# Optimization experiments

Measured on AMD Instinct MI355X. Metric: run time of the kernel, lower is better.

## Reference

```python
import jax, jax.numpy as jnp
import numpy as np

N = 100000   # nodes
E = 1600000  # edges (before self-loops)
C = 128      # num_node_features == graph_hidden_channels (residuals require equality)
NHID = 512
NOUT = 256
B = 512      # number of graphs in the batch
BN_EPS = 1e-5


def setup_inputs() -> dict:
    key = jax.random.key(0)
    ks = list(jax.random.split(key, 32))
    k = iter(ks)

    def w(shape, fan_in):
        return jax.random.normal(next(k), shape, jnp.float32) * (1.0 / np.sqrt(fan_in))

    inp = {}
    inp["x"] = jax.random.normal(next(k), (N, C), jnp.float32)
    inp["edge_index"] = jax.random.randint(next(k), (2, E), 0, N, jnp.int32)
    inp["batch"] = jnp.sort(jax.random.randint(next(k), (N,), 0, B, jnp.int32))
    # three GCN layers: lin weight [C,C], bias [C], BN gamma/beta
    for i in (1, 2, 3):
        inp[f"W{i}"] = w((C, C), C)
        inp[f"b{i}"] = jnp.zeros((C,), jnp.float32)
        inp[f"g{i}"] = jnp.ones((C,), jnp.float32)
        inp[f"be{i}"] = jnp.zeros((C,), jnp.float32)
    # GAT (1 head)
    inp["Wa"] = w((C, C), C)
    inp["asrc"] = w((C,), C)
    inp["adst"] = w((C,), C)
    inp["ba"] = jnp.zeros((C,), jnp.float32)
    inp["ga"] = jnp.ones((C,), jnp.float32)
    inp["bea"] = jnp.zeros((C,), jnp.float32)
    # MLP head
    inp["Wh1"] = w((C, NHID), C)
    inp["bh1"] = jnp.zeros((NHID,), jnp.float32)
    inp["Wm0"] = w((NHID, NHID), NHID)
    inp["bm0"] = jnp.zeros((NHID,), jnp.float32)
    inp["Wm1"] = w((NHID, NHID), NHID)
    inp["bm1"] = jnp.zeros((NHID,), jnp.float32)
    inp["Wo"] = w((NHID, NOUT), NHID)
    inp["bo"] = jnp.zeros((NOUT,), jnp.float32)
    return inp


def _add_self_loops(edge_index):
    loops = jnp.arange(N, dtype=edge_index.dtype)
    src = jnp.concatenate([edge_index[0], loops])
    dst = jnp.concatenate([edge_index[1], loops])
    return src, dst


def _gcn(x, src, dst, W, b):
    # PyG GCNConv: add self-loops, D^-1/2 (A+I) D^-1/2 (x W) + b
    deg = jax.ops.segment_sum(jnp.ones_like(dst, jnp.float32), dst, num_segments=N)
    dinv = jax.lax.rsqrt(jnp.maximum(deg, 1.0))
    norm = dinv[src] * dinv[dst]                      # [E+N]
    h = x @ W                                         # [N,C]
    msg = h[src] * norm[:, None]                      # gather + scale
    return jax.ops.segment_sum(msg, dst, num_segments=N) + b


def _gat(x, src, dst, W, asrc, adst, b):
    # PyG GATConv, heads=1: self-loops, alpha = softmax_dst(leaky_relu(a_s.h_j + a_d.h_i))
    h = x @ W                                         # [N,C]
    es = (h * asrc).sum(-1)                           # [N]
    ed = (h * adst).sum(-1)
    e = jax.nn.leaky_relu(es[src] + ed[dst], 0.2)     # [E+N]
    m = jax.ops.segment_max(e, dst, num_segments=N)
    ex = jnp.exp(e - m[dst])
    s = jax.ops.segment_sum(ex, dst, num_segments=N)
    alpha = ex / (s[dst] + 1e-16)
    out = jax.ops.segment_sum(h[src] * alpha[:, None], dst, num_segments=N)
    return out + b


def _bn(h, g, be):
    # BatchNorm in training mode: biased batch stats over node dim
    m = h.mean(0)
    v = ((h - m) ** 2).mean(0)
    return (h - m) * jax.lax.rsqrt(v + BN_EPS) * g + be


def reference(x, edge_index, batch,
              W1, b1, g1, be1, W2, b2, g2, be2, W3, b3, g3, be3,
              Wa, asrc, adst, ba, ga, bea,
              Wh1, bh1, Wm0, bm0, Wm1, bm1, Wo, bo):
    src, dst = _add_self_loops(edge_index)
    x = jax.nn.relu(_bn(_gcn(x, src, dst, W1, b1), g1, be1)) + x
    x = jax.nn.relu(_bn(_gcn(x, src, dst, W2, b2), g2, be2)) + x
    x = jax.nn.relu(_bn(_gcn(x, src, dst, W3, b3), g3, be3)) + x
    x = jax.nn.relu(_bn(_gat(x, src, dst, Wa, asrc, adst, ba), ga, bea)) + x
    # global mean pool over graphs
    sums = jax.ops.segment_sum(x, batch, num_segments=B)
    cnt = jax.ops.segment_sum(jnp.ones((N,), jnp.float32), batch, num_segments=B)
    x = sums / jnp.maximum(cnt, 1.0)[:, None]         # [B,C]
    x = jax.nn.relu(x @ Wh1 + bh1)
    x = jax.nn.relu(x @ Wm0 + bm0)
    x = jax.nn.relu(x @ Wm1 + bm1)
    return x @ Wo + bo                                # [B,NOUT]
```

## Files before the change

kernel.cpp:

```cpp
#include <hip/hip_runtime.h>

#define N_NODES 100000
#define N_EDGES 1600000
#define CCH     128
#define BG      512
#define NHID    512
#define NOUT    256
#define BN_EPS  1e-5f

typedef __attribute__((ext_vector_type(8))) short s16x8;
typedef __attribute__((ext_vector_type(4))) float f32x4;

static __device__ __forceinline__ float leaky(float x) { return x > 0.f ? x : 0.2f * x; }
static __device__ __forceinline__ uint32_t bfr16(float x) {
  uint32_t u = __float_as_uint(x);
  u += 0x7fffu + ((u >> 16) & 1u);
  return u >> 16;
}
static __device__ __forceinline__ uint32_t pack2(float a, float b) {
  return bfr16(a) | (bfr16(b) << 16);
}
static __device__ __forceinline__ float blo(uint32_t u) { return __uint_as_float(u << 16); }
static __device__ __forceinline__ float bhi(uint32_t u) { return __uint_as_float(u & 0xffff0000u); }

__global__ void hist_kernel(const int* __restrict__ dst, int* __restrict__ indeg) {
  int e = blockIdx.x * 256 + threadIdx.x;
  if (e < N_EDGES) atomicAdd(&indeg[dst[e]], 1);
}

__global__ __launch_bounds__(256) void scan_chunks(const int* __restrict__ indeg,
                                                   int* __restrict__ rowstart,
                                                   int* __restrict__ chunksum) {
  int tid = threadIdx.x;
  int base = blockIdx.x * 1024 + tid * 4;
  int4 v;
  if (base + 3 < N_NODES) {
    v = *(const int4*)(indeg + base);
  } else {
    v.x = (base + 0 < N_NODES) ? indeg[base + 0] : 0;
    v.y = (base + 1 < N_NODES) ? indeg[base + 1] : 0;
    v.z = (base + 2 < N_NODES) ? indeg[base + 2] : 0;
    v.w = (base + 3 < N_NODES) ? indeg[base + 3] : 0;
  }
  int s = v.x + v.y + v.z + v.w;
  __shared__ int ss[256];
  ss[tid] = s;
  __syncthreads();
  for (int off = 1; off < 256; off <<= 1) {
    int t = (tid >= off) ? ss[tid - off] : 0;
    __syncthreads();
    ss[tid] += t;
    __syncthreads();
  }
  int excl = ss[tid] - s;
  if (base + 0 < N_NODES) rowstart[base + 0] = excl;
  if (base + 1 < N_NODES) rowstart[base + 1] = excl + v.x;
  if (base + 2 < N_NODES) rowstart[base + 2] = excl + v.x + v.y;
  if (base + 3 < N_NODES) rowstart[base + 3] = excl + v.x + v.y + v.z;
  if (tid == 255) chunksum[blockIdx.x] = ss[255];
}

__global__ void scan_sums(int* __restrict__ chunksum, int nch) {
  __shared__ int ss[128];
  int tid = threadIdx.x;
  int v = (tid < nch) ? chunksum[tid] : 0;
  ss[tid] = v;
  __syncthreads();
  for (int off = 1; off < 128; off <<= 1) {
    int t = (tid >= off) ? ss[tid - off] : 0;
    __syncthreads();
    ss[tid] += t;
    __syncthreads();
  }
  if (tid < nch) chunksum[tid] = ss[tid] - v;
}

__global__ void scan_add(int* __restrict__ rowstart, const int* __restrict__ chunksum) {
  int i = blockIdx.x * 256 + threadIdx.x;
  if (i < N_NODES)      rowstart[i] += chunksum[i >> 10];
  else if (i == N_NODES) rowstart[N_NODES] = N_EDGES;
}

__global__ void compute_dinv(const int* __restrict__ indeg, float* __restrict__ dinv) {
  int i = blockIdx.x * 256 + threadIdx.x;
  if (i < N_NODES) dinv[i] = rsqrtf((float)(indeg[i] + 1));
}

__global__ void scatter_edges(const int* __restrict__ src, const int* __restrict__ dst,
                              const int* __restrict__ rowstart, int* __restrict__ cursor,
                              const float* __restrict__ dinv, int2* __restrict__ csr_sw) {
  int e = blockIdx.x * 256 + threadIdx.x;
  if (e < N_EDGES) {
    int d = dst[e];
    int s = src[e];
    int p = rowstart[d] + atomicAdd(&cursor[d], 1);
    float w = dinv[s] * dinv[d];
    csr_sw[p] = make_int2(s, __float_as_int(w));
  }
}

__global__ void cast_bf16_kernel(const float2* __restrict__ x2, uint32_t* __restrict__ xb) {
  size_t idx = (size_t)blockIdx.x * 256 + threadIdx.x;
  if (idx >= (size_t)N_NODES * 64) return;
  float2 v = x2[idx];
  xb[idx] = pack2(v.x, v.y);
}

__global__ void pack_w_kernel(const float* __restrict__ W, unsigned short* __restrict__ Wp) {
  int t = blockIdx.x * 256 + threadIdx.x;
  if (t >= 2048) return;
  int lane = t & 63;
  int ks = (t >> 6) & 3;
  int nt = t >> 8;
  int c = nt * 16 + (lane & 15);
  int kb = ks * 32 + (lane >> 4) * 8;
#pragma unroll
  for (int i = 0; i < 8; ++i)
    Wp[(size_t)t * 8 + i] = (unsigned short)bfr16(W[(size_t)(kb + i) * 128 + c]);
}

__global__ __launch_bounds__(256) void gemm_mfma(const uint32_t* __restrict__ Ab,
                                                 const unsigned short* __restrict__ Wp,
                                                 uint32_t* __restrict__ Hb,
                                                 int M) {
  int wave = threadIdx.x >> 6, lane = threadIdx.x & 63;
  int row0 = blockIdx.x * 128 + wave * 32;
  const unsigned short* A16 = (const unsigned short*)Ab;

  f32x4 acc[2][8];
#pragma unroll
  for (int mt = 0; mt < 2; ++mt)
#pragma unroll
    for (int nt = 0; nt < 8; ++nt) acc[mt][nt] = (f32x4){0.f, 0.f, 0.f, 0.f};

  s16x8 a[2][4];
  int r = lane & 15, ko = (lane >> 4) * 8;
#pragma unroll
  for (int mt = 0; mt < 2; ++mt) {
    int row = row0 + mt * 16 + r;
    bool v = row < M;
    const unsigned short* ap = A16 + (size_t)row * 128 + ko;
#pragma unroll
    for (int ks = 0; ks < 4; ++ks) {
      s16x8 af = {0, 0, 0, 0, 0, 0, 0, 0};
      if (v) af = *(const s16x8*)(ap + ks * 32);
      a[mt][ks] = af;
    }
  }
#pragma unroll
  for (int ks = 0; ks < 4; ++ks) {
#pragma unroll
    for (int nt = 0; nt < 8; ++nt) {
      s16x8 b = *(const s16x8*)(Wp + ((size_t)(nt * 4 + ks) * 64 + lane) * 8);
      acc[0][nt] = __builtin_amdgcn_mfma_f32_16x16x32_bf16(a[0][ks], b, acc[0][nt], 0, 0, 0);
      acc[1][nt] = __builtin_amdgcn_mfma_f32_16x16x32_bf16(a[1][ks], b, acc[1][nt], 0, 0, 0);
    }
  }
#pragma unroll
  for (int mt = 0; mt < 2; ++mt) {
#pragma unroll
    for (int nt = 0; nt < 8; ++nt) {
#pragma unroll
      for (int reg = 0; reg < 4; ++reg) {
        float v0 = acc[mt][nt][reg];
        float v1 = __shfl_xor(v0, 1);
        int row = row0 + mt * 16 + (lane >> 4) * 4 + reg;
        int col = nt * 16 + (lane & 15);
        if (!(lane & 1) && row < M)
          Hb[(size_t)row * 64 + (col >> 1)] = pack2(v0, v1);
      }
    }
  }
}

template <int GAT>
__global__ __launch_bounds__(256) void agg_kernel(const uint2* __restrict__ Hb2,
                                                  const int* __restrict__ rowstart,
                                                  const int2* __restrict__ pack,
                                                  const float* __restrict__ dinv,
                                                  const float* __restrict__ wselfa,
                                                  const float* __restrict__ winv,
                                                  float4* __restrict__ agg4,
                                                  float* __restrict__ stats) {
  int tid = threadIdx.x;
  int lane = tid & 63;
  int hl = lane & 31;
  int half = lane >> 5;
  int gw = (blockIdx.x * 256 + tid) >> 6;
  int nw = (gridDim.x * 256) >> 6;
  float s0 = 0, s1 = 0, s2 = 0, s3 = 0, q0 = 0, q1 = 0, q2 = 0, q3 = 0;
  for (int pi = gw; pi < N_NODES / 2; pi += nw) {
    int n = 2 * pi + half;
    int e0 = rowstart[n], e1 = rowstart[n + 1];
    int len = e1 - e0;
    int G = (len + 3) >> 2;
    int Gmax = max(G, __shfl_xor(G, 32));
    int ecl = (len > 0) ? (e1 - 1) : 0;
    float selfw, fscale;
    if (GAT) { selfw = wselfa[n]; fscale = winv[n]; }
    else     { float di = dinv[n]; selfw = di * di; fscale = 1.f; }
    uint2 hs = Hb2[(size_t)n * 32 + hl];
    float c0 = blo(hs.x) * selfw, c1 = bhi(hs.x) * selfw;
    float c2 = blo(hs.y) * selfw, c3 = bhi(hs.y) * selfw;

    if (Gmax > 0) {
      uint2 rA0, rA1, rA2, rA3;
      float wA0, wA1, wA2, wA3;
      int iB0, iB1, iB2, iB3;
      float wB0 = 0, wB1 = 0, wB2 = 0, wB3 = 0;
      iB0 = iB1 = iB2 = iB3 = 0;
      {
        int e = e0;
        int2 pa = pack[e < e1 ? e : ecl];
        int2 pb = pack[e + 1 < e1 ? e + 1 : ecl];
        int2 pc = pack[e + 2 < e1 ? e + 2 : ecl];
        int2 pd = pack[e + 3 < e1 ? e + 3 : ecl];
        wA0 = (e < e1) ? __int_as_float(pa.y) : 0.f;
        wA1 = (e + 1 < e1) ? __int_as_float(pb.y) : 0.f;
        wA2 = (e + 2 < e1) ? __int_as_float(pc.y) : 0.f;
        wA3 = (e + 3 < e1) ? __int_as_float(pd.y) : 0.f;
        rA0 = Hb2[(size_t)pa.x * 32 + hl];
        rA1 = Hb2[(size_t)pb.x * 32 + hl];
        rA2 = Hb2[(size_t)pc.x * 32 + hl];
        rA3 = Hb2[(size_t)pd.x * 32 + hl];
      }
      if (Gmax > 1) {
        int e = e0 + 4;
        int2 pa = pack[e < e1 ? e : ecl];
        int2 pb = pack[e + 1 < e1 ? e + 1 : ecl];
        int2 pc = pack[e + 2 < e1 ? e + 2 : ecl];
        int2 pd = pack[e + 3 < e1 ? e + 3 : ecl];
        iB0 = pa.x; wB0 = (e < e1) ? __int_as_float(pa.y) : 0.f;
        iB1 = pb.x; wB1 = (e + 1 < e1) ? __int_as_float(pb.y) : 0.f;
        iB2 = pc.x; wB2 = (e + 2 < e1) ? __int_as_float(pc.y) : 0.f;
        iB3 = pd.x; wB3 = (e + 3 < e1) ? __int_as_float(pd.y) : 0.f;
      }
      for (int g = 0; g < Gmax; ++g) {
        uint2 rB0, rB1, rB2, rB3;
        int nI0, nI1, nI2, nI3;
        float nw0, nw1, nw2, nw3;
        if (g + 1 < Gmax) {
          rB0 = Hb2[(size_t)iB0 * 32 + hl];
          rB1 = Hb2[(size_t)iB1 * 32 + hl];
          rB2 = Hb2[(size_t)iB2 * 32 + hl];
          rB3 = Hb2[(size_t)iB3 * 32 + hl];
        }
        if (g + 2 < Gmax) {
          int e = e0 + (g + 2) * 4;
          int2 pa = pack[e < e1 ? e : ecl];
          int2 pb = pack[e + 1 < e1 ? e + 1 : ecl];
          int2 pc = pack[e + 2 < e1 ? e + 2 : ecl];
          int2 pd = pack[e + 3 < e1 ? e + 3 : ecl];
          nI0 = pa.x; nw0 = (e < e1) ? __int_as_float(pa.y) : 0.f;
          nI1 = pb.x; nw1 = (e + 1 < e1) ? __int_as_float(pb.y) : 0.f;
          nI2 = pc.x; nw2 = (e + 2 < e1) ? __int_as_float(pc.y) : 0.f;
          nI3 = pd.x; nw3 = (e + 3 < e1) ? __int_as_float(pd.y) : 0.f;
        }
        c0 = fmaf(blo(rA0.x), wA0, c0); c1 = fmaf(bhi(rA0.x), wA0, c1);
        c2 = fmaf(blo(rA0.y), wA0, c2); c3 = fmaf(bhi(rA0.y), wA0, c3);
        c0 = fmaf(blo(rA1.x), wA1, c0); c1 = fmaf(bhi(rA1.x), wA1, c1);
        c2 = fmaf(blo(rA1.y), wA1, c2); c3 = fmaf(bhi(rA1.y), wA1, c3);
        c0 = fmaf(blo(rA2.x), wA2, c0); c1 = fmaf(bhi(rA2.x), wA2, c1);
        c2 = fmaf(blo(rA2.y), wA2, c2); c3 = fmaf(bhi(rA2.y), wA2, c3);
        c0 = fmaf(blo(rA3.x), wA3, c0); c1 = fmaf(bhi(rA3.x), wA3, c1);
        c2 = fmaf(blo(rA3.y), wA3, c2); c3 = fmaf(bhi(rA3.y), wA3, c3);
        rA0 = rB0; rA1 = rB1; rA2 = rB2; rA3 = rB3;
        wA0 = wB0; wA1 = wB1; wA2 = wB2; wA3 = wB3;
        iB0 = nI0; iB1 = nI1; iB2 = nI2; iB3 = nI3;
        wB0 = nw0; wB1 = nw1; wB2 = nw2; wB3 = nw3;
      }
    }
    if (GAT) { c0 *= fscale; c1 *= fscale; c2 *= fscale; c3 *= fscale; }
    agg4[(size_t)n * 32 + hl] = make_float4(c0, c1, c2, c3);
    s0 += c0; s1 += c1; s2 += c2; s3 += c3;
    q0 += c0 * c0; q1 += c1 * c1; q2 += c2 * c2; q3 += c3 * c3;
  }
  s0 += __shfl_xor(s0, 32); s1 += __shfl_xor(s1, 32);
  s2 += __shfl_xor(s2, 32); s3 += __shfl_xor(s3, 32);
  q0 += __shfl_xor(q0, 32); q1 += __shfl_xor(q1, 32);
  q2 += __shfl_xor(q2, 32); q3 += __shfl_xor(q3, 32);
  __shared__ float red[4][128];
  int w = tid >> 6;
  if (half == 0) {
    red[w][4 * hl + 0] = s0; red[w][4 * hl + 1] = s1;
    red[w][4 * hl + 2] = s2; red[w][4 * hl + 3] = s3;
  }
  __syncthreads();
  if (w == 0) {
    float a = red[0][2 * lane] + red[1][2 * lane] + red[2][2 * lane] + red[3][2 * lane];
    float b = red[0][2 * lane + 1] + red[1][2 * lane + 1] + red[2][2 * lane + 1] + red[3][2 * lane + 1];
    atomicAdd(&stats[2 * lane], a);
    atomicAdd(&stats[2 * lane + 1], b);
  }
  __syncthreads();
  if (half == 0) {
    red[w][4 * hl + 0] = q0; red[w][4 * hl + 1] = q1;
    red[w][4 * hl + 2] = q2; red[w][4 * hl + 3] = q3;
  }
  __syncthreads();
  if (w == 0) {
    float a = red[0][2 * lane] + red[1][2 * lane] + red[2][2 * lane] + red[3][2 * lane];
    float b = red[0][2 * lane + 1] + red[1][2 * lane + 1] + red[2][2 * lane + 1] + red[3][2 * lane + 1];
    atomicAdd(&stats[128 + 2 * lane], a);
    atomicAdd(&stats[128 + 2 * lane + 1], b);
  }
}

__global__ __launch_bounds__(256) void compute_esed(const uint32_t* __restrict__ Hb,
                                                    const float* __restrict__ asrc,
                                                    const float* __restrict__ adst,
                                                    float* __restrict__ es, float* __restrict__ ed) {
  int lane = threadIdx.x & 63;
  int gwave = (blockIdx.x * 256 + threadIdx.x) >> 6;
  if (gwave >= N_NODES) return;
  float2 av = ((const float2*)asrc)[lane];
  float2 dv = ((const float2*)adst)[lane];
  uint32_t hv = Hb[(size_t)gwave * 64 + lane];
  float hx = blo(hv), hy = bhi(hv);
  float e_s = hx * av.x + hy * av.y;
  float e_d = hx * dv.x + hy * dv.y;
  for (int off = 32; off; off >>= 1) {
    e_s += __shfl_down(e_s, off);
    e_d += __shfl_down(e_d, off);
  }
  if (lane == 0) { es[gwave] = e_s; ed[gwave] = e_d; }
}

__global__ void gat_prep_node(int2* __restrict__ pack, const int* __restrict__ rowstart,
                              const float* __restrict__ es, const float* __restrict__ ed,
                              float* __restrict__ wselfa, float* __restrict__ winv) {
  int n = blockIdx.x * 256 + threadIdx.x;
  if (n >= N_NODES) return;
  int e0 = rowstart[n], e1 = rowstart[n + 1];
  float edi = ed[n];
  float wself = __expf(leaky(es[n] + edi));
  float s = wself;
  for (int e = e0; e < e1; ++e) {
    int sidx = pack[e].x;
    float w = __expf(leaky(es[sidx] + edi));
    pack[e].y = __float_as_int(w);
    s += w;
  }
  wselfa[n] = wself;
  winv[n] = 1.f / (s + 1e-16f);
}

__global__ void bn_relu_res(const float4* __restrict__ agg4, const float* __restrict__ stats,
                            const float* __restrict__ gamma, const float* __restrict__ beta,
                            uint2* __restrict__ xb) {
  size_t idx = (size_t)blockIdx.x * 256 + threadIdx.x;
  if (idx >= (size_t)N_NODES * 32) return;
  int c = ((int)(idx & 31)) * 4;
  const float n_inv = 1.f / (float)N_NODES;
  float sc[4], bc[4];
#pragma unroll
  for (int k = 0; k < 4; ++k) {
    float m = stats[c + k] * n_inv;
    float v = stats[128 + c + k] * n_inv - m * m;
    sc[k] = gamma[c + k] * rsqrtf(v + BN_EPS);
    bc[k] = beta[c + k] - m * sc[k];
  }
  float4 a = agg4[idx];
  uint2 xi = xb[idx];
  float r0 = fmaxf(fmaf(a.x, sc[0], bc[0]), 0.f) + blo(xi.x);
  float r1 = fmaxf(fmaf(a.y, sc[1], bc[1]), 0.f) + bhi(xi.x);
  float r2 = fmaxf(fmaf(a.z, sc[2], bc[2]), 0.f) + blo(xi.y);
  float r3 = fmaxf(fmaf(a.w, sc[3], bc[3]), 0.f) + bhi(xi.y);
  xb[idx] = make_uint2(pack2(r0, r1), pack2(r2, r3));
}

__global__ void graph_starts(const int* __restrict__ batch, int* __restrict__ gstart) {
  int n = blockIdx.x * 256 + threadIdx.x;
  if (n >= N_NODES) return;
  int b = batch[n];
  int bp = (n == 0) ? -1 : batch[n - 1];
  for (int g = bp + 1; g <= b; ++g) gstart[g] = n;
  if (n == N_NODES - 1) {
    for (int g = b + 1; g <= BG; ++g) gstart[g] = N_NODES;
  }
}

__global__ __launch_bounds__(256) void pool_kernel(const uint32_t* __restrict__ xb,
                                                   const int* __restrict__ gstart,
                                                   float* __restrict__ pooled) {
  int g = blockIdx.x;
  int c = threadIdx.x & 127;
  int half = threadIdx.x >> 7;
  int s = gstart[g], e = gstart[g + 1];
  float acc = 0.f;
  for (int n = s + half; n < e; n += 2) {
    uint32_t u = xb[(size_t)n * 64 + (c >> 1)];
    acc += (c & 1) ? bhi(u) : blo(u);
  }
  __shared__ float red[256];
  red[threadIdx.x] = acc;
  __syncthreads();
  if (half == 0) {
    float v = red[c] + red[128 + c];
    int cnt = e - s;
    pooled[(size_t)g * 128 + c] = v / fmaxf((float)cnt, 1.f);
  }
}

template <int RELU, int BIAS>
__global__ __launch_bounds__(256) void gemm_f32(const float* __restrict__ A,
                                                const float* __restrict__ W,
                                                const float* __restrict__ bias,
                                                float* __restrict__ Cmat,
                                                int M, int K, int N) {
  __shared__ float As[32][128];
  __shared__ float Bs[32][128];
  int tid = threadIdx.x;
  int row0 = blockIdx.x * 128, col0 = blockIdx.y * 128;
  int tx = tid & 15, ty = tid >> 4;
  float acc[8][8];
#pragma unroll
  for (int i = 0; i < 8; ++i)
#pragma unroll
    for (int j = 0; j < 8; ++j) acc[i][j] = 0.f;

  for (int k0 = 0; k0 < K; k0 += 32) {
    {
      int r = tid >> 1;
      int kseg = (tid & 1) * 16;
      bool valid = (row0 + r) < M;
      const float* ap = A + (size_t)(row0 + r) * K + k0 + kseg;
#pragma unroll
      for (int q = 0; q < 4; ++q) {
        float4 v;
        if (valid) v = *(const float4*)(ap + q * 4);
        else { v.x = v.y = v.z = v.w = 0.f; }
        As[kseg + q * 4 + 0][r] = v.x;
        As[kseg + q * 4 + 1][r] = v.y;
        As[kseg + q * 4 + 2][r] = v.z;
        As[kseg + q * 4 + 3][r] = v.w;
      }
    }
    {
      int kk = tid >> 3;
      int seg = (tid & 7) * 16;
      const float* wp = W + (size_t)(k0 + kk) * N + col0 + seg;
#pragma unroll
      for (int q = 0; q < 4; ++q)
        *(float4*)&Bs[kk][seg + q * 4] = *(const float4*)(wp + q * 4);
    }
    __syncthreads();
#pragma unroll
    for (int kk = 0; kk < 32; ++kk) {
      float4 a0 = *(const float4*)&As[kk][ty * 4];
      float4 a1 = *(const float4*)&As[kk][64 + ty * 4];
      float4 b0 = *(const float4*)&Bs[kk][tx * 4];
      float4 b1 = *(const float4*)&Bs[kk][64 + tx * 4];
      float av[8] = {a0.x, a0.y, a0.z, a0.w, a1.x, a1.y, a1.z, a1.w};
      float bv[8] = {b0.x, b0.y, b0.z, b0.w, b1.x, b1.y, b1.z, b1.w};
#pragma unroll
      for (int i = 0; i < 8; ++i)
#pragma unroll
        for (int j = 0; j < 8; ++j) acc[i][j] = fmaf(av[i], bv[j], acc[i][j]);
    }
    __syncthreads();
  }
#pragma unroll
  for (int i = 0; i < 8; ++i) {
    int r = row0 + ((i < 4) ? (ty * 4 + i) : (64 + ty * 4 + i - 4));
    if (r >= M) continue;
#pragma unroll
    for (int j = 0; j < 8; ++j) {
      int c = col0 + ((j < 4) ? (tx * 4 + j) : (64 + tx * 4 + j - 4));
      float v = acc[i][j];
      if (BIAS) v += bias[c];
      if (RELU) v = fmaxf(v, 0.f);
      Cmat[(size_t)r * N + c] = v;
    }
  }
}

extern "C" void kernel_launch(void* const* d_in, const int* in_sizes, int n_in,
                              void* d_out, int out_size, void* d_ws, size_t ws_size,
                              hipStream_t stream) {
  const float* x_in  = (const float*)d_in[0];
  const int*   eidx  = (const int*)d_in[1];
  const int*   batch = (const int*)d_in[2];
  const float* W1 = (const float*)d_in[3];
  const float* g1 = (const float*)d_in[5];
  const float* be1 = (const float*)d_in[6];
  const float* W2 = (const float*)d_in[7];
  const float* g2 = (const float*)d_in[9];
  const float* be2 = (const float*)d_in[10];
  const float* W3 = (const float*)d_in[11];
  const float* g3 = (const float*)d_in[13];
  const float* be3 = (const float*)d_in[14];
  const float* Wa = (const float*)d_in[15];
  const float* asrc = (const float*)d_in[16];
  const float* adst = (const float*)d_in[17];
  const float* ga = (const float*)d_in[19];
  const float* bea = (const float*)d_in[20];
  const float* Wh1 = (const float*)d_in[21];
  const float* bh1 = (const float*)d_in[22];
  const float* Wm0 = (const float*)d_in[23];
  const float* bm0 = (const float*)d_in[24];
  const float* Wm1 = (const float*)d_in[25];
  const float* bm1 = (const float*)d_in[26];
  const float* Wo = (const float*)d_in[27];
  const float* bo = (const float*)d_in[28];

  const int* src = eidx;
  const int* dst = eidx + N_EDGES;

  char* p = (char*)d_ws;
  auto alloc = [&](size_t bytes) {
    char* r = p;
    p += (bytes + 255) & ~(size_t)255;
    return r;
  };
  uint32_t* Hb     = (uint32_t*)alloc((size_t)N_NODES * 64 * 4);
  uint32_t* xb     = (uint32_t*)alloc((size_t)N_NODES * 64 * 4);
  float* agg       = (float*)alloc((size_t)N_NODES * CCH * 4);
  int2*  csr_sw    = (int2*)alloc((size_t)N_EDGES * 8);
  int*   rowstart  = (int*)alloc((size_t)(N_NODES + 1) * 4);
  int*   indeg     = (int*)alloc((size_t)2 * N_NODES * 4);
  int*   cursor    = indeg + N_NODES;
  float* dinv      = (float*)alloc((size_t)N_NODES * 4);
  float* es        = (float*)alloc((size_t)N_NODES * 4);
  float* ed        = (float*)alloc((size_t)N_NODES * 4);
  float* wselfa    = (float*)alloc((size_t)N_NODES * 4);
  float* winv      = (float*)alloc((size_t)N_NODES * 4);
  int*   chunksum  = (int*)alloc(128 * 4);
  float* stats     = (float*)alloc(4 * 256 * 4);
  int*   gstart    = (int*)alloc((BG + 1) * 4);
  float* pooled    = (float*)alloc((size_t)BG * CCH * 4);
  float* m1        = (float*)alloc((size_t)BG * NHID * 4);
  float* m2        = (float*)alloc((size_t)BG * NHID * 4);
  unsigned short* Wp1 = (unsigned short*)alloc(2048 * 8 * 2);
  unsigned short* Wp2 = (unsigned short*)alloc(2048 * 8 * 2);
  unsigned short* Wp3 = (unsigned short*)alloc(2048 * 8 * 2);
  unsigned short* Wp4 = (unsigned short*)alloc(2048 * 8 * 2);

  hipMemsetAsync(indeg, 0, (size_t)2 * N_NODES * 4, stream);
  hipMemsetAsync(stats, 0, 4 * 256 * 4, stream);

  hist_kernel<<<(N_EDGES + 255) / 256, 256, 0, stream>>>(dst, indeg);
  scan_chunks<<<98, 256, 0, stream>>>(indeg, rowstart, chunksum);
  scan_sums<<<1, 128, 0, stream>>>(chunksum, 98);
  scan_add<<<(N_NODES + 256) / 256, 256, 0, stream>>>(rowstart, chunksum);
  compute_dinv<<<(N_NODES + 255) / 256, 256, 0, stream>>>(indeg, dinv);
  scatter_edges<<<(N_EDGES + 255) / 256, 256, 0, stream>>>(src, dst, rowstart, cursor, dinv, csr_sw);

  const int el2_blocks = (N_NODES * 64 + 255) / 256;
  const int el4_blocks = (N_NODES * 32 + 255) / 256;
  cast_bf16_kernel<<<el2_blocks, 256, 0, stream>>>((const float2*)x_in, xb);
  pack_w_kernel<<<8, 256, 0, stream>>>(W1, Wp1);
  pack_w_kernel<<<8, 256, 0, stream>>>(W2, Wp2);
  pack_w_kernel<<<8, 256, 0, stream>>>(W3, Wp3);
  pack_w_kernel<<<8, 256, 0, stream>>>(Wa, Wp4);

  const int gemm_blocks_m = (N_NODES + 127) / 128;
  const int AGG_BLOCKS = 2048;

  const unsigned short* Wps[3] = {Wp1, Wp2, Wp3};
  const float* gs[3] = {g1, g2, g3};
  const float* bes[3] = {be1, be2, be3};
  for (int l = 0; l < 3; ++l) {
    gemm_mfma<<<gemm_blocks_m, 256, 0, stream>>>(xb, Wps[l], Hb, N_NODES);
    agg_kernel<0><<<AGG_BLOCKS, 256, 0, stream>>>((const uint2*)Hb, rowstart, csr_sw, dinv,
                                                  nullptr, nullptr, (float4*)agg, stats + l * 256);
    bn_relu_res<<<el4_blocks, 256, 0, stream>>>((const float4*)agg, stats + l * 256,
                                                gs[l], bes[l], (uint2*)xb);
  }

  gemm_mfma<<<gemm_blocks_m, 256, 0, stream>>>(xb, Wp4, Hb, N_NODES);
  compute_esed<<<(N_NODES + 3) / 4, 256, 0, stream>>>(Hb, asrc, adst, es, ed);
  gat_prep_node<<<(N_NODES + 255) / 256, 256, 0, stream>>>(csr_sw, rowstart, es, ed, wselfa, winv);
  agg_kernel<1><<<AGG_BLOCKS, 256, 0, stream>>>((const uint2*)Hb, rowstart, csr_sw, nullptr,
                                                wselfa, winv, (float4*)agg, stats + 3 * 256);
  bn_relu_res<<<el4_blocks, 256, 0, stream>>>((const float4*)agg, stats + 3 * 256,
                                              ga, bea, (uint2*)xb);

  graph_starts<<<(N_NODES + 255) / 256, 256, 0, stream>>>(batch, gstart);
  pool_kernel<<<BG, 256, 0, stream>>>(xb, gstart, pooled);

  gemm_f32<1, 1><<<dim3(4, 4), 256, 0, stream>>>(pooled, Wh1, bh1, m1, BG, CCH, NHID);
  gemm_f32<1, 1><<<dim3(4, 4), 256, 0, stream>>>(m1, Wm0, bm0, m2, BG, NHID, NHID);
  gemm_f32<1, 1><<<dim3(4, 4), 256, 0, stream>>>(m2, Wm1, bm1, m1, BG, NHID, NHID);
  gemm_f32<0, 1><<<dim3(4, 2), 256, 0, stream>>>(m1, Wo, bo, (float*)d_out, BG, NHID, NOUT);
}
```

Before: 1.201 ms.

## Fuse BN/ReLU/residual into GEMM prologue and pooling, restructure GAT weights

Folds the BatchNorm+ReLU+residual pass into the next layer's MFMA GEMM prologue, and the last one into the pooling kernel, so the separate elementwise kernel that re-read agg and xb is gone. The GAT edge-weight prep is now a per-edge pass that stores es[src]. The aggregation kernel computes the exp/leaky weights and softmax denominator inline, which costs a second pass over each row's edges. Small setup kernels (scan_add with dinv, input cast with weight packing) are merged to cut launch count.

```diff
diff --git a/kernel.cpp b/kernel.cpp
--- a/kernel.cpp
+++ b/kernel.cpp
@@ -75,15 +75,15 @@
   if (tid < nch) chunksum[tid] = ss[tid] - v;
 }
 
-__global__ void scan_add(int* __restrict__ rowstart, const int* __restrict__ chunksum) {
+__global__ void scan_add_dinv(int* __restrict__ rowstart, const int* __restrict__ chunksum,
+                              const int* __restrict__ indeg, float* __restrict__ dinv) {
   int i = blockIdx.x * 256 + threadIdx.x;
-  if (i < N_NODES)      rowstart[i] += chunksum[i >> 10];
-  else if (i == N_NODES) rowstart[N_NODES] = N_EDGES;
-}
-
-__global__ void compute_dinv(const int* __restrict__ indeg, float* __restrict__ dinv) {
-  int i = blockIdx.x * 256 + threadIdx.x;
-  if (i < N_NODES) dinv[i] = rsqrtf((float)(indeg[i] + 1));
+  if (i < N_NODES) {
+    rowstart[i] += chunksum[i >> 10];
+    dinv[i] = rsqrtf((float)(indeg[i] + 1));
+  } else if (i == N_NODES) {
+    rowstart[N_NODES] = N_EDGES;
+  }
 }
 
 __global__ void scatter_edges(const int* __restrict__ src, const int* __restrict__ dst,
@@ -99,16 +99,23 @@
   }
 }
 
-__global__ void cast_bf16_kernel(const float2* __restrict__ x2, uint32_t* __restrict__ xb) {
-  size_t idx = (size_t)blockIdx.x * 256 + threadIdx.x;
-  if (idx >= (size_t)N_NODES * 64) return;
-  float2 v = x2[idx];
-  xb[idx] = pack2(v.x, v.y);
-}
-
-__global__ void pack_w_kernel(const float* __restrict__ W, unsigned short* __restrict__ Wp) {
-  int t = blockIdx.x * 256 + threadIdx.x;
-  if (t >= 2048) return;
+__global__ void prep_kernel(const float2* __restrict__ x2, uint32_t* __restrict__ xb,
+                            const float* __restrict__ W1, const float* __restrict__ W2,
+                            const float* __restrict__ W3, const float* __restrict__ W4,
+                            unsigned short* __restrict__ Wp1, unsigned short* __restrict__ Wp2,
+                            unsigned short* __restrict__ Wp3, unsigned short* __restrict__ Wp4) {
+  int b = blockIdx.x;
+  if (b < 25000) {
+    size_t idx = (size_t)b * 256 + threadIdx.x;
+    float2 v = x2[idx];
+    xb[idx] = pack2(v.x, v.y);
+    return;
+  }
+  int pb = b - 25000;
+  int wsel = pb >> 3;
+  int t = (pb & 7) * 256 + threadIdx.x;
+  const float* W = (wsel == 0) ? W1 : (wsel == 1) ? W2 : (wsel == 2) ? W3 : W4;
+  unsigned short* Wp = (wsel == 0) ? Wp1 : (wsel == 1) ? Wp2 : (wsel == 2) ? Wp3 : Wp4;
   int lane = t & 63;
   int ks = (t >> 6) & 3;
   int nt = t >> 8;
@@ -119,13 +126,31 @@
     Wp[(size_t)t * 8 + i] = (unsigned short)bfr16(W[(size_t)(kb + i) * 128 + c]);
 }
 
-__global__ __launch_bounds__(256) void gemm_mfma(const uint32_t* __restrict__ Ab,
+template <int FUSE>
+__global__ __launch_bounds__(256) void gemm_mfma(uint32_t* __restrict__ xbm,
+                                                 const float* __restrict__ aggf,
+                                                 const float* __restrict__ stats,
+                                                 const float* __restrict__ gamma,
+                                                 const float* __restrict__ beta,
                                                  const unsigned short* __restrict__ Wp,
                                                  uint32_t* __restrict__ Hb,
                                                  int M) {
+  __shared__ float scs[128], bcs[128];
+  if (FUSE) {
+    int t = threadIdx.x;
+    if (t < 128) {
+      const float n_inv = 1.f / (float)N_NODES;
+      float m = stats[t] * n_inv;
+      float v = stats[128 + t] * n_inv - m * m;
+      float s = gamma[t] * rsqrtf(v + BN_EPS);
+      scs[t] = s;
+      bcs[t] = beta[t] - m * s;
+    }
+    __syncthreads();
+  }
   int wave = threadIdx.x >> 6, lane = threadIdx.x & 63;
   int row0 = blockIdx.x * 128 + wave * 32;
-  const unsigned short* A16 = (const unsigned short*)Ab;
+  int r = lane & 15, g = lane >> 4;
 
   f32x4 acc[2][8];
 #pragma unroll
@@ -134,26 +159,52 @@
     for (int nt = 0; nt < 8; ++nt) acc[mt][nt] = (f32x4){0.f, 0.f, 0.f, 0.f};
 
   s16x8 a[2][4];
-  int r = lane & 15, ko = (lane >> 4) * 8;
 #pragma unroll
   for (int mt = 0; mt < 2; ++mt) {
     int row = row0 + mt * 16 + r;
     bool v = row < M;
-    const unsigned short* ap = A16 + (size_t)row * 128 + ko;
-#pragma unroll
-    for (int ks = 0; ks < 4; ++ks) {
-      s16x8 af = {0, 0, 0, 0, 0, 0, 0, 0};
-      if (v) af = *(const s16x8*)(ap + ks * 32);
-      a[mt][ks] = af;
+    if (FUSE) {
+#pragma unroll
+      for (int ks = 0; ks < 4; ++ks) {
+        int ch = ks * 32 + g * 8;
+        s16x8 af = {0, 0, 0, 0, 0, 0, 0, 0};
+        if (v) {
+          const float4* ap = (const float4*)(aggf + (size_t)row * 128 + ch);
+          float4 a0 = ap[0], a1 = ap[1];
+          uint4 xo = *(const uint4*)(xbm + (size_t)row * 64 + (ch >> 1));
+          float aa[8] = {a0.x, a0.y, a0.z, a0.w, a1.x, a1.y, a1.z, a1.w};
+          float xold[8] = {blo(xo.x), bhi(xo.x), blo(xo.y), bhi(xo.y),
+                           blo(xo.z), bhi(xo.z), blo(xo.w), bhi(xo.w)};
+          uint32_t pk[4];
+#pragma unroll
+          for (int jj = 0; jj < 4; ++jj) {
+            float r0v = fmaxf(fmaf(aa[2 * jj],     scs[ch + 2 * jj],     bcs[ch + 2 * jj]),     0.f) + xold[2 * jj];
+            float r1v = fmaxf(fmaf(aa[2 * jj + 1], scs[ch + 2 * jj + 1], bcs[ch + 2 * jj + 1]), 0.f) + xold[2 * jj + 1];
+            pk[jj] = pack2(r0v, r1v);
+          }
+          uint4 st = make_uint4(pk[0], pk[1], pk[2], pk[3]);
+          *(uint4*)(xbm + (size_t)row * 64 + (ch >> 1)) = st;
+          af = *(s16x8*)&st;
+        }
+        a[mt][ks] = af;
+      }
+    } else {
+      const unsigned short* ap = (const unsigned short*)xbm + (size_t)row * 128 + g * 8;
+#pragma unroll
+      for (int ks = 0; ks < 4; ++ks) {
+        s16x8 af = {0, 0, 0, 0, 0, 0, 0, 0};
+        if (v) af = *(const s16x8*)(ap + ks * 32);
+        a[mt][ks] = af;
+      }
     }
   }
 #pragma unroll
   for (int ks = 0; ks < 4; ++ks) {
 #pragma unroll
     for (int nt = 0; nt < 8; ++nt) {
-      s16x8 b = *(const s16x8*)(Wp + ((size_t)(nt * 4 + ks) * 64 + lane) * 8);
-      acc[0][nt] = __builtin_amdgcn_mfma_f32_16x16x32_bf16(a[0][ks], b, acc[0][nt], 0, 0, 0);
-      acc[1][nt] = __builtin_amdgcn_mfma_f32_16x16x32_bf16(a[1][ks], b, acc[1][nt], 0, 0, 0);
+      s16x8 bfr = *(const s16x8*)(Wp + ((size_t)(nt * 4 + ks) * 64 + lane) * 8);
+      acc[0][nt] = __builtin_amdgcn_mfma_f32_16x16x32_bf16(a[0][ks], bfr, acc[0][nt], 0, 0, 0);
+      acc[1][nt] = __builtin_amdgcn_mfma_f32_16x16x32_bf16(a[1][ks], bfr, acc[1][nt], 0, 0, 0);
     }
   }
 #pragma unroll
@@ -178,8 +229,8 @@
                                                   const int* __restrict__ rowstart,
                                                   const int2* __restrict__ pack,
                                                   const float* __restrict__ dinv,
-                                                  const float* __restrict__ wselfa,
-                                                  const float* __restrict__ winv,
+                                                  const float* __restrict__ es,
+                                                  const float* __restrict__ ed,
                                                   float4* __restrict__ agg4,
                                                   float* __restrict__ stats) {
   int tid = threadIdx.x;
@@ -196,9 +247,23 @@
     int G = (len + 3) >> 2;
     int Gmax = max(G, __shfl_xor(G, 32));
     int ecl = (len > 0) ? (e1 - 1) : 0;
-    float selfw, fscale;
-    if (GAT) { selfw = wselfa[n]; fscale = winv[n]; }
-    else     { float di = dinv[n]; selfw = di * di; fscale = 1.f; }
+    float edi = 0.f, selfw, fscale = 1.f;
+    if (GAT) {
+      edi = ed[n];
+      float wself = __expf(leaky(es[n] + edi));
+      float wsum = (hl == 0) ? wself : 0.f;
+      for (int e = e0 + hl; e < e1; e += 32)
+        wsum += __expf(leaky(__int_as_float(pack[e].y) + edi));
+#pragma unroll
+      for (int off = 16; off; off >>= 1) wsum += __shfl_xor(wsum, off);
+      fscale = 1.f / (wsum + 1e-16f);
+      selfw = wself;
+    } else {
+      float di = dinv[n];
+      selfw = di * di;
+    }
+#define EDGEW(py, ok) (GAT ? ((ok) ? __expf(leaky(__int_as_float(py) + edi)) : 0.f) \
+                           : ((ok) ? __int_as_float(py) : 0.f))
     uint2 hs = Hb2[(size_t)n * 32 + hl];
     float c0 = blo(hs.x) * selfw, c1 = bhi(hs.x) * selfw;
     float c2 = blo(hs.y) * selfw, c3 = bhi(hs.y) * selfw;
@@ -206,19 +271,18 @@
     if (Gmax > 0) {
       uint2 rA0, rA1, rA2, rA3;
       float wA0, wA1, wA2, wA3;
-      int iB0, iB1, iB2, iB3;
+      int iB0 = 0, iB1 = 0, iB2 = 0, iB3 = 0;
       float wB0 = 0, wB1 = 0, wB2 = 0, wB3 = 0;
-      iB0 = iB1 = iB2 = iB3 = 0;
       {
         int e = e0;
         int2 pa = pack[e < e1 ? e : ecl];
         int2 pb = pack[e + 1 < e1 ? e + 1 : ecl];
         int2 pc = pack[e + 2 < e1 ? e + 2 : ecl];
         int2 pd = pack[e + 3 < e1 ? e + 3 : ecl];
-        wA0 = (e < e1) ? __int_as_float(pa.y) : 0.f;
-        wA1 = (e + 1 < e1) ? __int_as_float(pb.y) : 0.f;
-        wA2 = (e + 2 < e1) ? __int_as_float(pc.y) : 0.f;
-        wA3 = (e + 3 < e1) ? __int_as_float(pd.y) : 0.f;
+        wA0 = EDGEW(pa.y, e < e1);
+        wA1 = EDGEW(pb.y, e + 1 < e1);
+        wA2 = EDGEW(pc.y, e + 2 < e1);
+        wA3 = EDGEW(pd.y, e + 3 < e1);
         rA0 = Hb2[(size_t)pa.x * 32 + hl];
         rA1 = Hb2[(size_t)pb.x * 32 + hl];
         rA2 = Hb2[(size_t)pc.x * 32 + hl];
@@ -230,10 +294,10 @@
         int2 pb = pack[e + 1 < e1 ? e + 1 : ecl];
         int2 pc = pack[e + 2 < e1 ? e + 2 : ecl];
         int2 pd = pack[e + 3 < e1 ? e + 3 : ecl];
-        iB0 = pa.x; wB0 = (e < e1) ? __int_as_float(pa.y) : 0.f;
-        iB1 = pb.x; wB1 = (e + 1 < e1) ? __int_as_float(pb.y) : 0.f;
-        iB2 = pc.x; wB2 = (e + 2 < e1) ? __int_as_float(pc.y) : 0.f;
-        iB3 = pd.x; wB3 = (e + 3 < e1) ? __int_as_float(pd.y) : 0.f;
+        iB0 = pa.x; wB0 = EDGEW(pa.y, e < e1);
+        iB1 = pb.x; wB1 = EDGEW(pb.y, e + 1 < e1);
+        iB2 = pc.x; wB2 = EDGEW(pc.y, e + 2 < e1);
+        iB3 = pd.x; wB3 = EDGEW(pd.y, e + 3 < e1);
       }
       for (int g = 0; g < Gmax; ++g) {
         uint2 rB0, rB1, rB2, rB3;
@@ -251,10 +315,10 @@
           int2 pb = pack[e + 1 < e1 ? e + 1 : ecl];
           int2 pc = pack[e + 2 < e1 ? e + 2 : ecl];
           int2 pd = pack[e + 3 < e1 ? e + 3 : ecl];
-          nI0 = pa.x; nw0 = (e < e1) ? __int_as_float(pa.y) : 0.f;
-          nI1 = pb.x; nw1 = (e + 1 < e1) ? __int_as_float(pb.y) : 0.f;
-          nI2 = pc.x; nw2 = (e + 2 < e1) ? __int_as_float(pc.y) : 0.f;
-          nI3 = pd.x; nw3 = (e + 3 < e1) ? __int_as_float(pd.y) : 0.f;
+          nI0 = pa.x; nw0 = EDGEW(pa.y, e < e1);
+          nI1 = pb.x; nw1 = EDGEW(pb.y, e + 1 < e1);
+          nI2 = pc.x; nw2 = EDGEW(pc.y, e + 2 < e1);
+          nI3 = pd.x; nw3 = EDGEW(pd.y, e + 3 < e1);
         }
         c0 = fmaf(blo(rA0.x), wA0, c0); c1 = fmaf(bhi(rA0.x), wA0, c1);
         c2 = fmaf(blo(rA0.y), wA0, c2); c3 = fmaf(bhi(rA0.y), wA0, c3);
@@ -270,6 +334,7 @@
         wB0 = nw0; wB1 = nw1; wB2 = nw2; wB3 = nw3;
       }
     }
+#undef EDGEW
     if (GAT) { c0 *= fscale; c1 *= fscale; c2 *= fscale; c3 *= fscale; }
     agg4[(size_t)n * 32 + hl] = make_float4(c0, c1, c2, c3);
     s0 += c0; s1 += c1; s2 += c2; s3 += c3;
@@ -326,47 +391,13 @@
   if (lane == 0) { es[gwave] = e_s; ed[gwave] = e_d; }
 }
 
-__global__ void gat_prep_node(int2* __restrict__ pack, const int* __restrict__ rowstart,
-                              const float* __restrict__ es, const float* __restrict__ ed,
-                              float* __restrict__ wselfa, float* __restrict__ winv) {
-  int n = blockIdx.x * 256 + threadIdx.x;
-  if (n >= N_NODES) return;
-  int e0 = rowstart[n], e1 = rowstart[n + 1];
-  float edi = ed[n];
-  float wself = __expf(leaky(es[n] + edi));
-  float s = wself;
-  for (int e = e0; e < e1; ++e) {
-    int sidx = pack[e].x;
-    float w = __expf(leaky(es[sidx] + edi));
-    pack[e].y = __float_as_int(w);
-    s += w;
-  }
-  wselfa[n] = wself;
-  winv[n] = 1.f / (s + 1e-16f);
-}
-
-__global__ void bn_relu_res(const float4* __restrict__ agg4, const float* __restrict__ stats,
-                            const float* __restrict__ gamma, const float* __restrict__ beta,
-                            uint2* __restrict__ xb) {
-  size_t idx = (size_t)blockIdx.x * 256 + threadIdx.x;
-  if (idx >= (size_t)N_NODES * 32) return;
-  int c = ((int)(idx & 31)) * 4;
-  const float n_inv = 1.f / (float)N_NODES;
-  float sc[4], bc[4];
-#pragma unroll
-  for (int k = 0; k < 4; ++k) {
-    float m = stats[c + k] * n_inv;
-    float v = stats[128 + c + k] * n_inv - m * m;
-    sc[k] = gamma[c + k] * rsqrtf(v + BN_EPS);
-    bc[k] = beta[c + k] - m * sc[k];
-  }
-  float4 a = agg4[idx];
-  uint2 xi = xb[idx];
-  float r0 = fmaxf(fmaf(a.x, sc[0], bc[0]), 0.f) + blo(xi.x);
-  float r1 = fmaxf(fmaf(a.y, sc[1], bc[1]), 0.f) + bhi(xi.x);
-  float r2 = fmaxf(fmaf(a.z, sc[2], bc[2]), 0.f) + blo(xi.y);
-  float r3 = fmaxf(fmaf(a.w, sc[3], bc[3]), 0.f) + bhi(xi.y);
-  xb[idx] = make_uint2(pack2(r0, r1), pack2(r2, r3));
+__global__ void gat_pack_kernel(int2* __restrict__ sw, const float* __restrict__ es) {
+  int e = blockIdx.x * 256 + threadIdx.x;
+  if (e < N_EDGES) {
+    int2 v = sw[e];
+    v.y = __float_as_int(es[v.x]);
+    sw[e] = v;
+  }
 }
 
 __global__ void graph_starts(const int* __restrict__ batch, int* __restrict__ gstart) {
@@ -380,25 +411,36 @@
   }
 }
 
-__global__ __launch_bounds__(256) void pool_kernel(const uint32_t* __restrict__ xb,
-                                                   const int* __restrict__ gstart,
-                                                   float* __restrict__ pooled) {
+__global__ __launch_bounds__(256) void pool_bn(const float* __restrict__ aggf,
+                                               const uint32_t* __restrict__ xb,
+                                               const float* __restrict__ stats,
+                                               const float* __restrict__ gamma,
+                                               const float* __restrict__ beta,
+                                               const int* __restrict__ gstart,
+                                               float* __restrict__ pooled) {
   int g = blockIdx.x;
   int c = threadIdx.x & 127;
   int half = threadIdx.x >> 7;
+  const float n_inv = 1.f / (float)N_NODES;
+  float m = stats[c] * n_inv;
+  float v = stats[128 + c] * n_inv - m * m;
+  float sc = gamma[c] * rsqrtf(v + BN_EPS);
+  float bc = beta[c] - m * sc;
   int s = gstart[g], e = gstart[g + 1];
   float acc = 0.f;
   for (int n = s + half; n < e; n += 2) {
+    float a = aggf[(size_t)n * 128 + c];
     uint32_t u = xb[(size_t)n * 64 + (c >> 1)];
-    acc += (c & 1) ? bhi(u) : blo(u);
+    float xo = (c & 1) ? bhi(u) : blo(u);
+    acc += fmaxf(fmaf(a, sc, bc), 0.f) + xo;
   }
   __shared__ float red[256];
   red[threadIdx.x] = acc;
   __syncthreads();
   if (half == 0) {
-    float v = red[c] + red[128 + c];
+    float vsum = red[c] + red[128 + c];
     int cnt = e - s;
-    pooled[(size_t)g * 128 + c] = v / fmaxf((float)cnt, 1.f);
+    pooled[(size_t)g * 128 + c] = vsum / fmaxf((float)cnt, 1.f);
   }
 }
 
@@ -523,8 +565,6 @@
   float* dinv      = (float*)alloc((size_t)N_NODES * 4);
   float* es        = (float*)alloc((size_t)N_NODES * 4);
   float* ed        = (float*)alloc((size_t)N_NODES * 4);
-  float* wselfa    = (float*)alloc((size_t)N_NODES * 4);
-  float* winv      = (float*)alloc((size_t)N_NODES * 4);
   int*   chunksum  = (int*)alloc(128 * 4);
   float* stats     = (float*)alloc(4 * 256 * 4);
   int*   gstart    = (int*)alloc((BG + 1) * 4);
@@ -542,42 +582,36 @@
   hist_kernel<<<(N_EDGES + 255) / 256, 256, 0, stream>>>(dst, indeg);
   scan_chunks<<<98, 256, 0, stream>>>(indeg, rowstart, chunksum);
   scan_sums<<<1, 128, 0, stream>>>(chunksum, 98);
-  scan_add<<<(N_NODES + 256) / 256, 256, 0, stream>>>(rowstart, chunksum);
-  compute_dinv<<<(N_NODES + 255) / 256, 256, 0, stream>>>(indeg, dinv);
+  scan_add_dinv<<<(N_NODES + 256) / 256, 256, 0, stream>>>(rowstart, chunksum, indeg, dinv);
   scatter_edges<<<(N_EDGES + 255) / 256, 256, 0, stream>>>(src, dst, rowstart, cursor, dinv, csr_sw);
 
-  const int el2_blocks = (N_NODES * 64 + 255) / 256;
-  const int el4_blocks = (N_NODES * 32 + 255) / 256;
-  cast_bf16_kernel<<<el2_blocks, 256, 0, stream>>>((const float2*)x_in, xb);
-  pack_w_kernel<<<8, 256, 0, stream>>>(W1, Wp1);
-  pack_w_kernel<<<8, 256, 0, stream>>>(W2, Wp2);
-  pack_w_kernel<<<8, 256, 0, stream>>>(W3, Wp3);
-  pack_w_kernel<<<8, 256, 0, stream>>>(Wa, Wp4);
+  prep_kernel<<<25000 + 32, 256, 0, stream>>>((const float2*)x_in, xb, W1, W2, W3, Wa,
+                                              Wp1, Wp2, Wp3, Wp4);
 
   const int gemm_blocks_m = (N_NODES + 127) / 128;
   const int AGG_BLOCKS = 2048;
 
-  const unsigned short* Wps[3] = {Wp1, Wp2, Wp3};
-  const float* gs[3] = {g1, g2, g3};
-  const float* bes[3] = {be1, be2, be3};
-  for (int l = 0; l < 3; ++l) {
-    gemm_mfma<<<gemm_blocks_m, 256, 0, stream>>>(xb, Wps[l], Hb, N_NODES);
-    agg_kernel<0><<<AGG_BLOCKS, 256, 0, stream>>>((const uint2*)Hb, rowstart, csr_sw, dinv,
-                                                  nullptr, nullptr, (float4*)agg, stats + l * 256);
-    bn_relu_res<<<el4_blocks, 256, 0, stream>>>((const float4*)agg, stats + l * 256,
-                                                gs[l], bes[l], (uint2*)xb);
-  }
-
-  gemm_mfma<<<gemm_blocks_m, 256, 0, stream>>>(xb, Wp4, Hb, N_NODES);
+  gemm_mfma<0><<<gemm_blocks_m, 256, 0, stream>>>(xb, nullptr, nullptr, nullptr, nullptr,
+                                                  Wp1, Hb, N_NODES);
+  agg_kernel<0><<<AGG_BLOCKS, 256, 0, stream>>>((const uint2*)Hb, rowstart, csr_sw, dinv,
+                                                nullptr, nullptr, (float4*)agg, stats + 0 * 256);
+  gemm_mfma<1><<<gemm_blocks_m, 256, 0, stream>>>(xb, agg, stats + 0 * 256, g1, be1,
+                                                  Wp2, Hb, N_NODES);
+  agg_kernel<0><<<AGG_BLOCKS, 256, 0, stream>>>((const uint2*)Hb, rowstart, csr_sw, dinv,
+                                                nullptr, nullptr, (float4*)agg, stats + 1 * 256);
+  gemm_mfma<1><<<gemm_blocks_m, 256, 0, stream>>>(xb, agg, stats + 1 * 256, g2, be2,
+                                                  Wp3, Hb, N_NODES);
+  agg_kernel<0><<<AGG_BLOCKS, 256, 0, stream>>>((const uint2*)Hb, rowstart, csr_sw, dinv,
+                                                nullptr, nullptr, (float4*)agg, stats + 2 * 256);
+  gemm_mfma<1><<<gemm_blocks_m, 256, 0, stream>>>(xb, agg, stats + 2 * 256, g3, be3,
+                                                  Wp4, Hb, N_NODES);
   compute_esed<<<(N_NODES + 3) / 4, 256, 0, stream>>>(Hb, asrc, adst, es, ed);
-  gat_prep_node<<<(N_NODES + 255) / 256, 256, 0, stream>>>(csr_sw, rowstart, es, ed, wselfa, winv);
+  gat_pack_kernel<<<(N_EDGES + 255) / 256, 256, 0, stream>>>(csr_sw, es);
   agg_kernel<1><<<AGG_BLOCKS, 256, 0, stream>>>((const uint2*)Hb, rowstart, csr_sw, nullptr,
-                                                wselfa, winv, (float4*)agg, stats + 3 * 256);
-  bn_relu_res<<<el4_blocks, 256, 0, stream>>>((const float4*)agg, stats + 3 * 256,
-                                              ga, bea, (uint2*)xb);
+                                                es, ed, (float4*)agg, stats + 3 * 256);
 
   graph_starts<<<(N_NODES + 255) / 256, 256, 0, stream>>>(batch, gstart);
-  pool_kernel<<<BG, 256, 0, stream>>>(xb, gstart, pooled);
+  pool_bn<<<BG, 256, 0, stream>>>(agg, xb, stats + 3 * 256, ga, bea, gstart, pooled);
 
   gemm_f32<1, 1><<<dim3(4, 4), 256, 0, stream>>>(pooled, Wh1, bh1, m1, BG, CCH, NHID);
   gemm_f32<1, 1><<<dim3(4, 4), 256, 0, stream>>>(m1, Wm0, bm0, m2, BG, NHID, NHID);
```

After: 1.158 ms. -3.6%, faster.
